# Optimization experiments

Hardware: AMD Instinct MI355X
Metric: run time of the kernel (lower is better)

## Reference

```python
import jax, jax.numpy as jnp
import numpy as np

B, S, H, NH = 2, 2048, 2048, 16
HD = H // NH

def setup_inputs() -> dict:
    key = jax.random.key(0)
    ks = jax.random.split(key, 6)
    scale = 1.0 / np.sqrt(H)
    return {
        "x": jax.random.normal(ks[0], (B, S, H), dtype=jnp.float32),
        "Wq": jax.random.normal(ks[1], (H, H), dtype=jnp.float32) * scale,
        "Wk": jax.random.normal(ks[2], (H, H), dtype=jnp.float32) * scale,
        "Wv": jax.random.normal(ks[3], (H, H), dtype=jnp.float32) * scale,
        "Wo": jax.random.normal(ks[4], (H, H), dtype=jnp.float32) * scale,
        "bo": jax.random.normal(ks[5], (H,), dtype=jnp.float32) * 0.01,
    }

def reference(x, Wq, Wk, Wv, Wo, bo):
    # nn.Linear convention: y = x @ W.T (W is [out, in])
    q = (x @ Wq.T).reshape(B, S, NH, HD).transpose(0, 2, 1, 3)  # [B,NH,S,HD]
    k = (x @ Wk.T).reshape(B, S, NH, HD).transpose(0, 2, 1, 3)
    v = (x @ Wv.T).reshape(B, S, NH, HD).transpose(0, 2, 1, 3)
    scale = jnp.asarray(HD, x.dtype) ** -0.5
    scores = jnp.einsum('bhqd,bhkd->bhqk', q, k) * scale  # [B,NH,S,S]
    attn = jax.nn.softmax(scores, axis=-1)
    out = jnp.einsum('bhqk,bhkd->bhqd', attn, v)  # [B,NH,S,HD]
    out = out.transpose(0, 2, 1, 3).reshape(B, S, H)
    return out @ Wo.T + bo
```

## Files before the change

### kernel.cpp

```cpp
#include <hip/hip_runtime.h>
#include <hip/hip_bf16.h>
#include <stdint.h>

#define S_LEN 2048
#define NHEADS 16
#define HDIM 128
#define H_TOT 2048
#define BATCH 2
#define M_TOK 4096
#define KDIM 2048

typedef __attribute__((ext_vector_type(8))) short bf16x8;
typedef __attribute__((ext_vector_type(4))) float f32x4;
typedef __attribute__((ext_vector_type(16))) float f32x16;

__device__ inline ushort bf16rn(float f) {
  union { float f; uint32_t u; } x; x.f = f;
  uint32_t r = x.u + 0x7FFF + ((x.u >> 16) & 1);
  return (ushort)(r >> 16);
}

__global__ __launch_bounds__(256) void cvt_bf16_kernel(const float* __restrict__ in,
                                                       ushort* __restrict__ out, int n4) {
  int i = blockIdx.x * blockDim.x + threadIdx.x;
  int stride = gridDim.x * blockDim.x;
  for (; i < n4; i += stride) {
    float4 v = reinterpret_cast<const float4*>(in)[i];
    ushort4 o;
    o.x = bf16rn(v.x); o.y = bf16rn(v.y); o.z = bf16rn(v.z); o.w = bf16rn(v.w);
    reinterpret_cast<ushort4*>(out)[i] = o;
  }
}

__global__ __launch_bounds__(256) void cvt4_bf16_kernel(const float* __restrict__ w0,
                                                        const float* __restrict__ w1,
                                                        const float* __restrict__ w2,
                                                        const float* __restrict__ w3,
                                                        ushort* __restrict__ o0,
                                                        ushort* __restrict__ o1,
                                                        ushort* __restrict__ o2,
                                                        ushort* __restrict__ o3) {
  const int N4 = KDIM * KDIM / 4;
  int i = blockIdx.x * blockDim.x + threadIdx.x;
  int stride = gridDim.x * blockDim.x;
  for (; i < 4 * N4; i += stride) {
    int seg = i >> 20, off = i & (N4 - 1);
    const float* in = (seg == 0) ? w0 : (seg == 1) ? w1 : (seg == 2) ? w2 : w3;
    ushort* out = (seg == 0) ? o0 : (seg == 1) ? o1 : (seg == 2) ? o2 : o3;
    float4 v = reinterpret_cast<const float4*>(in)[off];
    ushort4 o;
    o.x = bf16rn(v.x); o.y = bf16rn(v.y); o.z = bf16rn(v.z); o.w = bf16rn(v.w);
    reinterpret_cast<ushort4*>(out)[off] = o;
  }
}

template<int MODE, int NBX>
__global__ __launch_bounds__(512) void gemm2(const ushort* __restrict__ A,
                                             const ushort* __restrict__ Bw,
                                             void* __restrict__ C0,
                                             void* __restrict__ C1,
                                             void* __restrict__ C2,
                                             const float* __restrict__ bias,
                                             float scale) {
  __shared__ __attribute__((aligned(16))) char lds[3 * 49152];
  const int K = KDIM;
  const int NKT = K / 64;
  int tid = threadIdx.x;
  int wave = tid >> 6, lane = tid & 63;
  int lanelo = lane & 15, lanehi = lane >> 4;
  int wr = wave >> 2, wc = wave & 3;

  int bid = blockIdx.x;
  const int CHX = NBX / 8;
  int ii = bid >> 3;
  int bx = (bid & 7) * CHX + (ii % CHX);
  int by = ii / CHX;
  int bm = by * 128, bn = bx * 256;

  const ushort* srcA[2];
  const ushort* srcB[4];
#pragma unroll
  for (int i = 0; i < 2; i++) {
    int c = i * 512 + tid, row = c >> 3, slot = c & 7;
    srcA[i] = A + (size_t)(bm + row) * K + ((slot ^ (row & 7)) * 8);
  }
#pragma unroll
  for (int i = 0; i < 4; i++) {
    int c = i * 512 + tid, row = c >> 3, slot = c & 7;
    srcB[i] = Bw + (size_t)(bn + row) * K + ((slot ^ (row & 7)) * 8);
  }

#define STAGE(tile, buf)                                                                    \
  {                                                                                         \
    char* dA = lds + (buf) * 49152 + (size_t)tid * 16;                                      \
    char* dB = lds + (buf) * 49152 + 16384 + (size_t)tid * 16;                              \
    _Pragma("unroll") for (int i_ = 0; i_ < 2; i_++)                                        \
      __builtin_amdgcn_global_load_lds(                                                     \
          (const __attribute__((address_space(1))) void*)(srcA[i_] + (tile) * 64),          \
          (__attribute__((address_space(3))) void*)(dA + i_ * 8192), 16, 0, 0);             \
    _Pragma("unroll") for (int i_ = 0; i_ < 4; i_++)                                        \
      __builtin_amdgcn_global_load_lds(                                                     \
          (const __attribute__((address_space(1))) void*)(srcB[i_] + (tile) * 64),          \
          (__attribute__((address_space(3))) void*)(dB + i_ * 8192), 16, 0, 0);             \
  }

  f32x4 acc[4][4];
#pragma unroll
  for (int i = 0; i < 4; i++)
#pragma unroll
    for (int j = 0; j < 4; j++) acc[i][j] = (f32x4){0.f, 0.f, 0.f, 0.f};

  STAGE(0, 0);
  STAGE(1, 1);
  asm volatile("s_waitcnt vmcnt(6)" ::: "memory");
  __builtin_amdgcn_s_barrier();
  __builtin_amdgcn_sched_barrier(0);

  for (int t = 0; t < NKT; t++) {
    STAGE((t + 2) & (NKT - 1), (t + 2) % 3);

    const ushort* bufc = (const ushort*)(lds + (t % 3) * 49152);

    bf16x8 bfr[4][2];
#pragma unroll
    for (int nf = 0; nf < 4; nf++)
#pragma unroll
      for (int kh = 0; kh < 2; kh++) {
        int row = wc * 64 + nf * 16 + lanelo;
        int slot = (kh * 4 + lanehi) ^ (row & 7);
        bfr[nf][kh] = *reinterpret_cast<const bf16x8*>(&bufc[8192 + row * 64 + slot * 8]);
      }

    __builtin_amdgcn_s_setprio(1);
#pragma unroll
    for (int mf = 0; mf < 4; mf++) {
      int row = wr * 64 + mf * 16 + lanelo;
      bf16x8 af[2];
#pragma unroll
      for (int kh = 0; kh < 2; kh++) {
        int slot = (kh * 4 + lanehi) ^ (row & 7);
        af[kh] = *reinterpret_cast<const bf16x8*>(&bufc[row * 64 + slot * 8]);
      }
#pragma unroll
      for (int nf = 0; nf < 4; nf++)
#pragma unroll
        for (int kh = 0; kh < 2; kh++)
          acc[mf][nf] = __builtin_amdgcn_mfma_f32_16x16x32_bf16(af[kh], bfr[nf][kh],
                                                                acc[mf][nf], 0, 0, 0);
    }
    __builtin_amdgcn_s_setprio(0);

    asm volatile("s_waitcnt vmcnt(6)" ::: "memory");
    __builtin_amdgcn_s_barrier();
    __builtin_amdgcn_sched_barrier(0);
  }

  if (MODE == 2) {
    float* Cf = (float*)C0;
#pragma unroll
    for (int nf = 0; nf < 4; nf++) {
      int n = bn + wc * 64 + nf * 16 + lanelo;
      float bv = bias[n];
#pragma unroll
      for (int mf = 0; mf < 4; mf++)
#pragma unroll
        for (int q = 0; q < 4; q++) {
          int m = bm + wr * 64 + mf * 16 + lanehi * 4 + q;
          Cf[(size_t)m * H_TOT + n] = acc[mf][nf][q] + bv;
        }
    }
  } else {
    int seg = bn >> 11;
    ushort* dst = (seg == 0) ? (ushort*)C0 : (seg == 1) ? (ushort*)C1 : (ushort*)C2;
    float sc = (seg == 0) ? scale : 1.0f;
#pragma unroll
    for (int nf = 0; nf < 4; nf++) {
      int n = (bn & 2047) + wc * 64 + nf * 16 + lanelo;
      int h = n >> 7, d = n & 127;
#pragma unroll
      for (int mf = 0; mf < 4; mf++)
#pragma unroll
        for (int q = 0; q < 4; q++) {
          int m = bm + wr * 64 + mf * 16 + lanehi * 4 + q;
          int b = m >> 11, s = m & 2047;
          int bh = b * NHEADS + h;
          size_t idx;
          if (seg < 2) {
            idx = (((size_t)(bh * 64 + (s >> 5)) * 8 + (d >> 4)) * 64 +
                   ((d >> 3) & 1) * 32 + (s & 31)) * 8 + (d & 7);
          } else {
            int r = s & 15;
            int e = (r & 3) | ((r >> 1) & 4);
            int hi = (r >> 2) & 1;
            idx = (((size_t)(bh * 64 + (s >> 5)) * 8 + ((s >> 4) & 1) * 4 + (d >> 5)) * 64 +
                   hi * 32 + (d & 31)) * 8 + e;
          }
          dst[idx] = bf16rn(acc[mf][nf][q] * sc);
        }
    }
  }
#undef STAGE
}

__global__ __launch_bounds__(128) void attn_kernel(const ushort* __restrict__ Qf,
                                                   const ushort* __restrict__ Kf,
                                                   const ushort* __restrict__ Vf,
                                                   ushort* __restrict__ Ob) {
  __shared__ __attribute__((aligned(16))) ushort KV[2][8192];
  __shared__ float lsinv[2][32];
  int lane = threadIdx.x & 63, wave = threadIdx.x >> 6;
  int hi = lane >> 5;

  int bid = blockIdx.x;
  int swz = (bid & 7) * 128 + (bid >> 3);
  int bh = swz >> 5, qt = swz & 31;
  int b = bh >> 4, h = bh & 15;
  int qrow0 = qt * 64 + wave * 32;

  const bf16x8* Qv = reinterpret_cast<const bf16x8*>(Qf) +
                     ((size_t)(bh * 64 + qt * 2 + wave) * 8) * 64 + lane;
  bf16x8 qf[8];
#pragma unroll
  for (int kc = 0; kc < 8; kc++) qf[kc] = Qv[kc * 64];

  f32x16 oacc[4];
#pragma unroll
  for (int d32 = 0; d32 < 4; d32++)
#pragma unroll
    for (int r = 0; r < 16; r++) oacc[d32][r] = 0.f;
  float lsum = 0.f;
  int laneoff = lane * 8;
  const ushort* sbase = wave ? Vf : Kf;

#define STAGE(kt, bufsel)                                                                   \
  {                                                                                         \
    size_t gc = ((size_t)(bh * 64 + (kt))) * 8;                                             \
    _Pragma("unroll") for (int i_ = 0; i_ < 8; i_++) {                                      \
      __builtin_amdgcn_global_load_lds(                                                     \
          (const __attribute__((address_space(1))) void*)(sbase + (gc + i_) * 512 + laneoff),\
          (__attribute__((address_space(3))) void*)(&KV[bufsel][(wave * 8 + i_) * 512]),    \
          16, 0, 0);                                                                        \
    }                                                                                       \
  }

  union pu { bf16x8 v; uint32_t u[4]; };
  pu paA0, paA1, paB0, paB1;
  bf16x8 vrA[8], vrB[8];
  const bf16x8 bz = {0, 0, 0, 0, 0, 0, 0, 0};
#pragma unroll
  for (int j = 0; j < 4; j++) { paA0.u[j] = 0; paA1.u[j] = 0; }
#pragma unroll
  for (int i = 0; i < 8; i++) vrA[i] = bz;

  STAGE(0, 0);
  asm volatile("s_waitcnt vmcnt(0)" ::: "memory");
  __syncthreads();

  const int NT = S_LEN / 32;

#define BODY(T, PI0, PI1, VI, PO0, PO1, VO)                                                 \
  {                                                                                         \
    if ((T) + 1 < NT) STAGE((T) + 1, ((T) + 1) & 1);                                        \
    const ushort* lb = &KV[(T) & 1][0];                                                     \
    f32x16 S;                                                                               \
    _Pragma("unroll") for (int r = 0; r < 16; r++) S[r] = 0.f;                              \
    __builtin_amdgcn_s_setprio(1);                                                          \
    _Pragma("unroll") for (int kc = 0; kc < 8; kc++) {                                      \
      bf16x8 kfr = *reinterpret_cast<const bf16x8*>(&lb[kc * 512 + laneoff]);               \
      S = __builtin_amdgcn_mfma_f32_32x32x16_bf16(kfr, qf[kc], S, 0, 0, 0);                 \
    }                                                                                       \
    _Pragma("unroll") for (int d32 = 0; d32 < 4; d32++) {                                   \
      oacc[d32] = __builtin_amdgcn_mfma_f32_32x32x16_bf16(PI0.v, VI[d32], oacc[d32], 0, 0, 0); \
      oacc[d32] = __builtin_amdgcn_mfma_f32_32x32x16_bf16(PI1.v, VI[4 + d32], oacc[d32], 0, 0, 0); \
    }                                                                                       \
    __builtin_amdgcn_s_setprio(0);                                                          \
    float p_[16];                                                                           \
    _Pragma("unroll") for (int r = 0; r < 16; r++) { p_[r] = exp2f(S[r]); lsum += p_[r]; }  \
    _Pragma("unroll") for (int j = 0; j < 4; j++) {                                         \
      uint32_t w0_, w1_;                                                                    \
      asm("v_cvt_pk_bf16_f32 %0, %1, %2" : "=v"(w0_) : "v"(p_[2 * j]), "v"(p_[2 * j + 1])); \
      asm("v_cvt_pk_bf16_f32 %0, %1, %2" : "=v"(w1_) : "v"(p_[8 + 2 * j]), "v"(p_[9 + 2 * j])); \
      PO0.u[j] = w0_; PO1.u[j] = w1_;                                                       \
    }                                                                                       \
    _Pragma("unroll") for (int i_ = 0; i_ < 8; i_++)                                        \
      VO[i_] = *reinterpret_cast<const bf16x8*>(&lb[4096 + i_ * 512 + laneoff]);            \
    asm volatile("s_waitcnt vmcnt(0)" ::: "memory");                                        \
    __syncthreads();                                                                        \
  }

  for (int t = 0; t < NT; t += 2) {
    BODY(t,     paA0, paA1, vrA, paB0, paB1, vrB);
    BODY(t + 1, paB0, paB1, vrB, paA0, paA1, vrA);
  }
#pragma unroll
  for (int d32 = 0; d32 < 4; d32++) {
    oacc[d32] = __builtin_amdgcn_mfma_f32_32x32x16_bf16(paA0.v, vrA[d32], oacc[d32], 0, 0, 0);
    oacc[d32] = __builtin_amdgcn_mfma_f32_32x32x16_bf16(paA1.v, vrA[4 + d32], oacc[d32], 0, 0, 0);
  }

  float total = lsum + __shfl_xor(lsum, 32);
  if (lane < 32) lsinv[wave][lane] = 1.0f / total;
  __syncthreads();

  float ls[16];
#pragma unroll
  for (int r = 0; r < 16; r++) ls[r] = lsinv[wave][(r & 3) + 8 * (r >> 2) + 4 * hi];
#pragma unroll
  for (int d32 = 0; d32 < 4; d32++)
#pragma unroll
    for (int r = 0; r < 16; r++) {
      int row = (r & 3) + 8 * (r >> 2) + 4 * hi;
      size_t idx = ((size_t)(b * S_LEN + qrow0 + row)) * H_TOT + h * HDIM + d32 * 32 + (lane & 31);
      Ob[idx] = bf16rn(oacc[d32][r] * ls[r]);
    }
#undef BODY
#undef STAGE
}

extern "C" void kernel_launch(void* const* d_in, const int* in_sizes, int n_in,
                              void* d_out, int out_size, void* d_ws, size_t ws_size,
                              hipStream_t stream) {
  const float* x  = (const float*)d_in[0];
  const float* Wq = (const float*)d_in[1];
  const float* Wk = (const float*)d_in[2];
  const float* Wv = (const float*)d_in[3];
  const float* Wo = (const float*)d_in[4];
  const float* bo = (const float*)d_in[5];
  float* out = (float*)d_out;

  char* w = (char*)d_ws;
  ushort* xb  = (ushort*)w; w += (size_t)M_TOK * KDIM * 2;
  ushort* Wqb = (ushort*)w; w += (size_t)KDIM * KDIM * 2;
  ushort* Wkb = (ushort*)w; w += (size_t)KDIM * KDIM * 2;
  ushort* Wvb = (ushort*)w; w += (size_t)KDIM * KDIM * 2;
  ushort* Wob = (ushort*)w; w += (size_t)KDIM * KDIM * 2;
  ushort* Qh  = (ushort*)w; w += (size_t)M_TOK * KDIM * 2;
  ushort* Kh  = (ushort*)w; w += (size_t)M_TOK * KDIM * 2;
  ushort* Vt  = (ushort*)w; w += (size_t)M_TOK * KDIM * 2;
  ushort* Ob  = (ushort*)w; w += (size_t)M_TOK * KDIM * 2;

  hipLaunchKernelGGL(cvt_bf16_kernel, dim3(2048), dim3(256), 0, stream, x, xb, M_TOK * KDIM / 4);
  hipLaunchKernelGGL(cvt4_bf16_kernel, dim3(2048), dim3(256), 0, stream,
                     Wq, Wk, Wv, Wo, Wqb, Wkb, Wvb, Wob);

  const float sl = 0.08838834764831845f * 1.4426950408889634f;

  hipLaunchKernelGGL((gemm2<0, 24>), dim3(768), dim3(512), 0, stream,
                     xb, Wqb, (void*)Qh, (void*)Kh, (void*)Vt, (const float*)nullptr, sl);

  hipLaunchKernelGGL(attn_kernel, dim3(1024), dim3(128), 0, stream, Qh, Kh, Vt, Ob);

  hipLaunchKernelGGL((gemm2<2, 8>), dim3(256), dim3(512), 0, stream,
                     Ob, Wob, (void*)out, nullptr, nullptr, bo, 1.0f);
}
```

Baseline: 271.0 us.

## Restructure GEMM to 4-wave blocks with K-tile 32 and configurable N width

Replaces the 8-wave, 128x256, K=64 GEMM with a 4-wave kernel using a K-tile of 32 and a templated N width. The QKV projection keeps 128x256 tiles, and the output projection moves to 128x128 tiles on a 512-block grid. Launch bounds request two blocks per CU, and the LDS XOR swizzle is dropped in favour of precomputed fragment offsets. The aim is higher occupancy and cheaper address arithmetic, at the cost of more barriers per K step, possible LDS bank conflicts without the swizzle, and higher register use per wave.

```diff
diff --git a/kernel.cpp b/kernel.cpp
--- a/kernel.cpp
+++ b/kernel.cpp
@@ -54,103 +54,101 @@
   }
 }
 
-template<int MODE, int NBX>
-__global__ __launch_bounds__(512) void gemm2(const ushort* __restrict__ A,
-                                             const ushort* __restrict__ Bw,
-                                             void* __restrict__ C0,
-                                             void* __restrict__ C1,
-                                             void* __restrict__ C2,
-                                             const float* __restrict__ bias,
-                                             float scale) {
-  __shared__ __attribute__((aligned(16))) char lds[3 * 49152];
+template<int MODE, int NF, int NBX>
+__global__ __launch_bounds__(256, 2) void gemm3(const ushort* __restrict__ A,
+                                                const ushort* __restrict__ Bw,
+                                                void* __restrict__ C0,
+                                                void* __restrict__ C1,
+                                                void* __restrict__ C2,
+                                                const float* __restrict__ bias,
+                                                float scale) {
+  const int BN = NF * 32;
+  const int BUFB = (128 + BN) * 64;
+  const int NGL = (128 + BN) / 64;
+  __shared__ __attribute__((aligned(16))) char lds[3 * (128 + NF * 32) * 64];
   const int K = KDIM;
-  const int NKT = K / 64;
+  const int NKT = K / 32;
   int tid = threadIdx.x;
   int wave = tid >> 6, lane = tid & 63;
   int lanelo = lane & 15, lanehi = lane >> 4;
-  int wr = wave >> 2, wc = wave & 3;
+  int wr = wave >> 1, wc = wave & 1;
 
   int bid = blockIdx.x;
   const int CHX = NBX / 8;
   int ii = bid >> 3;
   int bx = (bid & 7) * CHX + (ii % CHX);
   int by = ii / CHX;
-  int bm = by * 128, bn = bx * 256;
-
-  const ushort* srcA[2];
-  const ushort* srcB[4];
-#pragma unroll
-  for (int i = 0; i < 2; i++) {
-    int c = i * 512 + tid, row = c >> 3, slot = c & 7;
-    srcA[i] = A + (size_t)(bm + row) * K + ((slot ^ (row & 7)) * 8);
-  }
-#pragma unroll
-  for (int i = 0; i < 4; i++) {
-    int c = i * 512 + tid, row = c >> 3, slot = c & 7;
-    srcB[i] = Bw + (size_t)(bn + row) * K + ((slot ^ (row & 7)) * 8);
+  int bm = by * 128, bn = bx * BN;
+
+  const ushort* src[NGL];
+#pragma unroll
+  for (int i = 0; i < NGL; i++) {
+    int c = i * 256 + tid;
+    if (c < 512) {
+      int row = c >> 2, slot = c & 3;
+      src[i] = A + (size_t)(bm + row) * K + slot * 8;
+    } else {
+      int c2 = c - 512;
+      int row = c2 >> 2, slot = c2 & 3;
+      src[i] = Bw + (size_t)(bn + row) * K + slot * 8;
+    }
   }
 
 #define STAGE(tile, buf)                                                                    \
   {                                                                                         \
-    char* dA = lds + (buf) * 49152 + (size_t)tid * 16;                                      \
-    char* dB = lds + (buf) * 49152 + 16384 + (size_t)tid * 16;                              \
-    _Pragma("unroll") for (int i_ = 0; i_ < 2; i_++)                                        \
+    char* d = lds + (buf) * BUFB + (size_t)tid * 16;                                        \
+    _Pragma("unroll") for (int i_ = 0; i_ < NGL; i_++)                                      \
       __builtin_amdgcn_global_load_lds(                                                     \
-          (const __attribute__((address_space(1))) void*)(srcA[i_] + (tile) * 64),          \
-          (__attribute__((address_space(3))) void*)(dA + i_ * 8192), 16, 0, 0);             \
-    _Pragma("unroll") for (int i_ = 0; i_ < 4; i_++)                                        \
-      __builtin_amdgcn_global_load_lds(                                                     \
-          (const __attribute__((address_space(1))) void*)(srcB[i_] + (tile) * 64),          \
-          (__attribute__((address_space(3))) void*)(dB + i_ * 8192), 16, 0, 0);             \
-  }
-
-  f32x4 acc[4][4];
+          (const __attribute__((address_space(1))) void*)(src[i_] + (tile) * 32),           \
+          (__attribute__((address_space(3))) void*)(d + i_ * 4096), 16, 0, 0);              \
+  }
+#define WAITCNT()                                                                           \
+  {                                                                                         \
+    if constexpr (NGL == 6) asm volatile("s_waitcnt vmcnt(6)" ::: "memory");                \
+    else asm volatile("s_waitcnt vmcnt(4)" ::: "memory");                                   \
+  }
+
+  f32x4 acc[4][NF];
 #pragma unroll
   for (int i = 0; i < 4; i++)
 #pragma unroll
-    for (int j = 0; j < 4; j++) acc[i][j] = (f32x4){0.f, 0.f, 0.f, 0.f};
+    for (int j = 0; j < NF; j++) acc[i][j] = (f32x4){0.f, 0.f, 0.f, 0.f};
+
+  int fo = lanelo * 64 + lanehi * 16;
+  int aoff[4], boff[NF];
+#pragma unroll
+  for (int mf = 0; mf < 4; mf++) aoff[mf] = (wr * 64 + mf * 16) * 64 + fo;
+#pragma unroll
+  for (int nf = 0; nf < NF; nf++) boff[nf] = 128 * 64 + (wc * NF * 16 + nf * 16) * 64 + fo;
 
   STAGE(0, 0);
   STAGE(1, 1);
-  asm volatile("s_waitcnt vmcnt(6)" ::: "memory");
+  WAITCNT();
   __builtin_amdgcn_s_barrier();
   __builtin_amdgcn_sched_barrier(0);
 
   for (int t = 0; t < NKT; t++) {
     STAGE((t + 2) & (NKT - 1), (t + 2) % 3);
 
-    const ushort* bufc = (const ushort*)(lds + (t % 3) * 49152);
-
-    bf16x8 bfr[4][2];
-#pragma unroll
-    for (int nf = 0; nf < 4; nf++)
-#pragma unroll
-      for (int kh = 0; kh < 2; kh++) {
-        int row = wc * 64 + nf * 16 + lanelo;
-        int slot = (kh * 4 + lanehi) ^ (row & 7);
-        bfr[nf][kh] = *reinterpret_cast<const bf16x8*>(&bufc[8192 + row * 64 + slot * 8]);
-      }
+    const char* bufc = lds + (t % 3) * BUFB;
+    bf16x8 bfr[NF], afr[4];
+#pragma unroll
+    for (int nf = 0; nf < NF; nf++)
+      bfr[nf] = *reinterpret_cast<const bf16x8*>(bufc + boff[nf]);
+#pragma unroll
+    for (int mf = 0; mf < 4; mf++)
+      afr[mf] = *reinterpret_cast<const bf16x8*>(bufc + aoff[mf]);
 
     __builtin_amdgcn_s_setprio(1);
 #pragma unroll
-    for (int mf = 0; mf < 4; mf++) {
-      int row = wr * 64 + mf * 16 + lanelo;
-      bf16x8 af[2];
-#pragma unroll
-      for (int kh = 0; kh < 2; kh++) {
-        int slot = (kh * 4 + lanehi) ^ (row & 7);
-        af[kh] = *reinterpret_cast<const bf16x8*>(&bufc[row * 64 + slot * 8]);
-      }
-#pragma unroll
-      for (int nf = 0; nf < 4; nf++)
-#pragma unroll
-        for (int kh = 0; kh < 2; kh++)
-          acc[mf][nf] = __builtin_amdgcn_mfma_f32_16x16x32_bf16(af[kh], bfr[nf][kh],
-                                                                acc[mf][nf], 0, 0, 0);
-    }
+    for (int mf = 0; mf < 4; mf++)
+#pragma unroll
+      for (int nf = 0; nf < NF; nf++)
+        acc[mf][nf] = __builtin_amdgcn_mfma_f32_16x16x32_bf16(afr[mf], bfr[nf],
+                                                              acc[mf][nf], 0, 0, 0);
     __builtin_amdgcn_s_setprio(0);
 
-    asm volatile("s_waitcnt vmcnt(6)" ::: "memory");
+    WAITCNT();
     __builtin_amdgcn_s_barrier();
     __builtin_amdgcn_sched_barrier(0);
   }
@@ -158,8 +156,8 @@
   if (MODE == 2) {
     float* Cf = (float*)C0;
 #pragma unroll
-    for (int nf = 0; nf < 4; nf++) {
-      int n = bn + wc * 64 + nf * 16 + lanelo;
+    for (int nf = 0; nf < NF; nf++) {
+      int n = bn + wc * NF * 16 + nf * 16 + lanelo;
       float bv = bias[n];
 #pragma unroll
       for (int mf = 0; mf < 4; mf++)
@@ -174,8 +172,8 @@
     ushort* dst = (seg == 0) ? (ushort*)C0 : (seg == 1) ? (ushort*)C1 : (ushort*)C2;
     float sc = (seg == 0) ? scale : 1.0f;
 #pragma unroll
-    for (int nf = 0; nf < 4; nf++) {
-      int n = (bn & 2047) + wc * 64 + nf * 16 + lanelo;
+    for (int nf = 0; nf < NF; nf++) {
+      int n = (bn & 2047) + wc * NF * 16 + nf * 16 + lanelo;
       int h = n >> 7, d = n & 127;
 #pragma unroll
       for (int mf = 0; mf < 4; mf++)
@@ -200,6 +198,7 @@
     }
   }
 #undef STAGE
+#undef WAITCNT
 }
 
 __global__ __launch_bounds__(128) void attn_kernel(const ushort* __restrict__ Qf,
@@ -345,11 +344,11 @@
 
   const float sl = 0.08838834764831845f * 1.4426950408889634f;
 
-  hipLaunchKernelGGL((gemm2<0, 24>), dim3(768), dim3(512), 0, stream,
+  hipLaunchKernelGGL((gemm3<0, 8, 24>), dim3(768), dim3(256), 0, stream,
                      xb, Wqb, (void*)Qh, (void*)Kh, (void*)Vt, (const float*)nullptr, sl);
 
   hipLaunchKernelGGL(attn_kernel, dim3(1024), dim3(128), 0, stream, Qh, Kh, Vt, Ob);
 
-  hipLaunchKernelGGL((gemm2<2, 8>), dim3(256), dim3(512), 0, stream,
+  hipLaunchKernelGGL((gemm3<2, 4, 16>), dim3(512), dim3(256), 0, stream,
                      Ob, Wob, (void*)out, nullptr, nullptr, bo, 1.0f);
 }
```

After: 276.6 us. 2.1% more time.

## Process two query tiles per wave and triple-buffer K/V in LDS

Applied to the files above, without the earlier changes.

Each wave now handles 64 query rows (two 32-row MFMA tiles), so every K and V fragment read from LDS feeds twice as many MFMAs, and the grid is halved to 512 blocks. V fragments are no longer kept in registers across iterations. Instead, a third LDS buffer lets the delayed P·V step reread V from the previous stage's buffer. This cuts LDS traffic per flop and register pressure from the V prefetch, but it doubles the accumulator registers, which may lower occupancy, and leaves fewer blocks to fill the CUs.

```diff
diff --git a/kernel.cpp b/kernel.cpp
--- a/kernel.cpp
+++ b/kernel.cpp
@@ -206,29 +206,29 @@
                                                    const ushort* __restrict__ Kf,
                                                    const ushort* __restrict__ Vf,
                                                    ushort* __restrict__ Ob) {
-  __shared__ __attribute__((aligned(16))) ushort KV[2][8192];
-  __shared__ float lsinv[2][32];
+  __shared__ __attribute__((aligned(16))) ushort KV[3][8192];
+  __shared__ float lsinv[4][32];
   int lane = threadIdx.x & 63, wave = threadIdx.x >> 6;
   int hi = lane >> 5;
 
   int bid = blockIdx.x;
-  int swz = (bid & 7) * 128 + (bid >> 3);
-  int bh = swz >> 5, qt = swz & 31;
+  int swz = (bid & 7) * 64 + (bid >> 3);
+  int bh = swz >> 4, qt = swz & 15;
   int b = bh >> 4, h = bh & 15;
-  int qrow0 = qt * 64 + wave * 32;
+  int qrow0 = qt * 128 + wave * 64;
 
   const bf16x8* Qv = reinterpret_cast<const bf16x8*>(Qf) +
-                     ((size_t)(bh * 64 + qt * 2 + wave) * 8) * 64 + lane;
-  bf16x8 qf[8];
-#pragma unroll
-  for (int kc = 0; kc < 8; kc++) qf[kc] = Qv[kc * 64];
-
-  f32x16 oacc[4];
+                     ((size_t)(bh * 64 + qt * 4 + wave * 2) * 8) * 64 + lane;
+  bf16x8 qf0[8], qf1[8];
+#pragma unroll
+  for (int kc = 0; kc < 8; kc++) { qf0[kc] = Qv[kc * 64]; qf1[kc] = Qv[(8 + kc) * 64]; }
+
+  f32x16 oacc0[4], oacc1[4];
 #pragma unroll
   for (int d32 = 0; d32 < 4; d32++)
 #pragma unroll
-    for (int r = 0; r < 16; r++) oacc[d32][r] = 0.f;
-  float lsum = 0.f;
+    for (int r = 0; r < 16; r++) { oacc0[d32][r] = 0.f; oacc1[d32][r] = 0.f; }
+  float lsum0 = 0.f, lsum1 = 0.f;
   int laneoff = lane * 8;
   const ushort* sbase = wave ? Vf : Kf;
 
@@ -244,13 +244,18 @@
   }
 
   union pu { bf16x8 v; uint32_t u[4]; };
-  pu paA0, paA1, paB0, paB1;
-  bf16x8 vrA[8], vrB[8];
-  const bf16x8 bz = {0, 0, 0, 0, 0, 0, 0, 0};
-#pragma unroll
-  for (int j = 0; j < 4; j++) { paA0.u[j] = 0; paA1.u[j] = 0; }
-#pragma unroll
-  for (int i = 0; i < 8; i++) vrA[i] = bz;
+  pu pA00, pA01, pA10, pA11, pB00, pB01, pB10, pB11;
+#pragma unroll
+  for (int j = 0; j < 4; j++) {
+    pA00.u[j] = 0; pA01.u[j] = 0; pA10.u[j] = 0; pA11.u[j] = 0;
+  }
+
+  {
+    const bf16x8 bz = {0, 0, 0, 0, 0, 0, 0, 0};
+#pragma unroll
+    for (int i = 0; i < 4; i++)
+      *reinterpret_cast<bf16x8*>(&KV[2][4096 + ((int)threadIdx.x * 4 + i) * 8]) = bz;
+  }
 
   STAGE(0, 0);
   asm volatile("s_waitcnt vmcnt(0)" ::: "memory");
@@ -258,60 +263,89 @@
 
   const int NT = S_LEN / 32;
 
-#define BODY(T, PI0, PI1, VI, PO0, PO1, VO)                                                 \
+#define BODY(T, PI00, PI01, PI10, PI11, PO00, PO01, PO10, PO11)                             \
   {                                                                                         \
-    if ((T) + 1 < NT) STAGE((T) + 1, ((T) + 1) & 1);                                        \
-    const ushort* lb = &KV[(T) & 1][0];                                                     \
-    f32x16 S;                                                                               \
-    _Pragma("unroll") for (int r = 0; r < 16; r++) S[r] = 0.f;                              \
+    if ((T) + 1 < NT) STAGE((T) + 1, ((T) + 1) % 3);                                        \
+    const ushort* lb = &KV[(T) % 3][0];                                                     \
+    const ushort* lbp = &KV[((T) + 2) % 3][0];                              \
+    f32x16 S0, S1;                                                                          \
+    _Pragma("unroll") for (int r = 0; r < 16; r++) { S0[r] = 0.f; S1[r] = 0.f; }            \
     __builtin_amdgcn_s_setprio(1);                                                          \
     _Pragma("unroll") for (int kc = 0; kc < 8; kc++) {                                      \
       bf16x8 kfr = *reinterpret_cast<const bf16x8*>(&lb[kc * 512 + laneoff]);               \
-      S = __builtin_amdgcn_mfma_f32_32x32x16_bf16(kfr, qf[kc], S, 0, 0, 0);                 \
+      S0 = __builtin_amdgcn_mfma_f32_32x32x16_bf16(kfr, qf0[kc], S0, 0, 0, 0);              \
+      S1 = __builtin_amdgcn_mfma_f32_32x32x16_bf16(kfr, qf1[kc], S1, 0, 0, 0);              \
     }                                                                                       \
     _Pragma("unroll") for (int d32 = 0; d32 < 4; d32++) {                                   \
-      oacc[d32] = __builtin_amdgcn_mfma_f32_32x32x16_bf16(PI0.v, VI[d32], oacc[d32], 0, 0, 0); \
-      oacc[d32] = __builtin_amdgcn_mfma_f32_32x32x16_bf16(PI1.v, VI[4 + d32], oacc[d32], 0, 0, 0); \
+      bf16x8 v0 = *reinterpret_cast<const bf16x8*>(&lbp[4096 + d32 * 512 + laneoff]);       \
+      bf16x8 v1 = *reinterpret_cast<const bf16x8*>(&lbp[4096 + (4 + d32) * 512 + laneoff]); \
+      oacc0[d32] = __builtin_amdgcn_mfma_f32_32x32x16_bf16(PI00.v, v0, oacc0[d32], 0, 0, 0);\
+      oacc0[d32] = __builtin_amdgcn_mfma_f32_32x32x16_bf16(PI01.v, v1, oacc0[d32], 0, 0, 0);\
+      oacc1[d32] = __builtin_amdgcn_mfma_f32_32x32x16_bf16(PI10.v, v0, oacc1[d32], 0, 0, 0);\
+      oacc1[d32] = __builtin_amdgcn_mfma_f32_32x32x16_bf16(PI11.v, v1, oacc1[d32], 0, 0, 0);\
     }                                                                                       \
     __builtin_amdgcn_s_setprio(0);                                                          \
-    float p_[16];                                                                           \
-    _Pragma("unroll") for (int r = 0; r < 16; r++) { p_[r] = exp2f(S[r]); lsum += p_[r]; }  \
     _Pragma("unroll") for (int j = 0; j < 4; j++) {                                         \
-      uint32_t w0_, w1_;                                                                    \
-      asm("v_cvt_pk_bf16_f32 %0, %1, %2" : "=v"(w0_) : "v"(p_[2 * j]), "v"(p_[2 * j + 1])); \
-      asm("v_cvt_pk_bf16_f32 %0, %1, %2" : "=v"(w1_) : "v"(p_[8 + 2 * j]), "v"(p_[9 + 2 * j])); \
-      PO0.u[j] = w0_; PO1.u[j] = w1_;                                                       \
+      float a0 = exp2f(S0[2 * j]), a1 = exp2f(S0[2 * j + 1]);                               \
+      float b0 = exp2f(S0[8 + 2 * j]), b1 = exp2f(S0[9 + 2 * j]);                           \
+      lsum0 += (a0 + a1) + (b0 + b1);                                                       \
+      uint32_t wa, wb;                                                                      \
+      asm("v_cvt_pk_bf16_f32 %0, %1, %2" : "=v"(wa) : "v"(a0), "v"(a1));                    \
+      asm("v_cvt_pk_bf16_f32 %0, %1, %2" : "=v"(wb) : "v"(b0), "v"(b1));                    \
+      PO00.u[j] = wa; PO01.u[j] = wb;                                                       \
+      float c0 = exp2f(S1[2 * j]), c1 = exp2f(S1[2 * j + 1]);                               \
+      float d0 = exp2f(S1[8 + 2 * j]), d1 = exp2f(S1[9 + 2 * j]);                           \
+      lsum1 += (c0 + c1) + (d0 + d1);                                                       \
+      uint32_t wc_, wd;                                                                     \
+      asm("v_cvt_pk_bf16_f32 %0, %1, %2" : "=v"(wc_) : "v"(c0), "v"(c1));                   \
+      asm("v_cvt_pk_bf16_f32 %0, %1, %2" : "=v"(wd) : "v"(d0), "v"(d1));                    \
+      PO10.u[j] = wc_; PO11.u[j] = wd;                                                      \
     }                                                                                       \
-    _Pragma("unroll") for (int i_ = 0; i_ < 8; i_++)                                        \
-      VO[i_] = *reinterpret_cast<const bf16x8*>(&lb[4096 + i_ * 512 + laneoff]);            \
     asm volatile("s_waitcnt vmcnt(0)" ::: "memory");                                        \
     __syncthreads();                                                                        \
   }
 
   for (int t = 0; t < NT; t += 2) {
-    BODY(t,     paA0, paA1, vrA, paB0, paB1, vrB);
-    BODY(t + 1, paB0, paB1, vrB, paA0, paA1, vrA);
-  }
-#pragma unroll
-  for (int d32 = 0; d32 < 4; d32++) {
-    oacc[d32] = __builtin_amdgcn_mfma_f32_32x32x16_bf16(paA0.v, vrA[d32], oacc[d32], 0, 0, 0);
-    oacc[d32] = __builtin_amdgcn_mfma_f32_32x32x16_bf16(paA1.v, vrA[4 + d32], oacc[d32], 0, 0, 0);
-  }
-
-  float total = lsum + __shfl_xor(lsum, 32);
-  if (lane < 32) lsinv[wave][lane] = 1.0f / total;
+    BODY(t,     pA00, pA01, pA10, pA11, pB00, pB01, pB10, pB11);
+    BODY(t + 1, pB00, pB01, pB10, pB11, pA00, pA01, pA10, pA11);
+  }
+  {
+    const ushort* lbp = &KV[(NT - 1) % 3][0];
+#pragma unroll
+    for (int d32 = 0; d32 < 4; d32++) {
+      bf16x8 v0 = *reinterpret_cast<const bf16x8*>(&lbp[4096 + d32 * 512 + laneoff]);
+      bf16x8 v1 = *reinterpret_cast<const bf16x8*>(&lbp[4096 + (4 + d32) * 512 + laneoff]);
+      oacc0[d32] = __builtin_amdgcn_mfma_f32_32x32x16_bf16(pA00.v, v0, oacc0[d32], 0, 0, 0);
+      oacc0[d32] = __builtin_amdgcn_mfma_f32_32x32x16_bf16(pA01.v, v1, oacc0[d32], 0, 0, 0);
+      oacc1[d32] = __builtin_amdgcn_mfma_f32_32x32x16_bf16(pA10.v, v0, oacc1[d32], 0, 0, 0);
+      oacc1[d32] = __builtin_amdgcn_mfma_f32_32x32x16_bf16(pA11.v, v1, oacc1[d32], 0, 0, 0);
+    }
+  }
+
+  float t0 = lsum0 + __shfl_xor(lsum0, 32);
+  float t1 = lsum1 + __shfl_xor(lsum1, 32);
+  if (lane < 32) {
+    lsinv[wave * 2 + 0][lane] = 1.0f / t0;
+    lsinv[wave * 2 + 1][lane] = 1.0f / t1;
+  }
   __syncthreads();
 
-  float ls[16];
-#pragma unroll
-  for (int r = 0; r < 16; r++) ls[r] = lsinv[wave][(r & 3) + 8 * (r >> 2) + 4 * hi];
+  float ls0[16], ls1[16];
+#pragma unroll
+  for (int r = 0; r < 16; r++) {
+    int row = (r & 3) + 8 * (r >> 2) + 4 * hi;
+    ls0[r] = lsinv[wave * 2 + 0][row];
+    ls1[r] = lsinv[wave * 2 + 1][row];
+  }
 #pragma unroll
   for (int d32 = 0; d32 < 4; d32++)
 #pragma unroll
     for (int r = 0; r < 16; r++) {
       int row = (r & 3) + 8 * (r >> 2) + 4 * hi;
-      size_t idx = ((size_t)(b * S_LEN + qrow0 + row)) * H_TOT + h * HDIM + d32 * 32 + (lane & 31);
-      Ob[idx] = bf16rn(oacc[d32][r] * ls[r]);
+      size_t idx0 = ((size_t)(b * S_LEN + qrow0 + row)) * H_TOT + h * HDIM + d32 * 32 + (lane & 31);
+      size_t idx1 = ((size_t)(b * S_LEN + qrow0 + 32 + row)) * H_TOT + h * HDIM + d32 * 32 + (lane & 31);
+      Ob[idx0] = bf16rn(oacc0[d32][r] * ls0[r]);
+      Ob[idx1] = bf16rn(oacc1[d32][r] * ls1[r]);
     }
 #undef BODY
 #undef STAGE
@@ -348,7 +382,7 @@
   hipLaunchKernelGGL((gemm2<0, 24>), dim3(768), dim3(512), 0, stream,
                      xb, Wqb, (void*)Qh, (void*)Kh, (void*)Vt, (const float*)nullptr, sl);
 
-  hipLaunchKernelGGL(attn_kernel, dim3(1024), dim3(128), 0, stream, Qh, Kh, Vt, Ob);
+  hipLaunchKernelGGL(attn_kernel, dim3(512), dim3(128), 0, stream, Qh, Kh, Vt, Ob);
 
   hipLaunchKernelGGL((gemm2<2, 8>), dim3(256), dim3(512), 0, stream,
                      Ob, Wob, (void*)out, nullptr, nullptr, bo, 1.0f);
```

Result: slower. 288.5 us (+6.5%).
